# Optimization experiments

Measured on AMD Instinct MI355X. Metric: run time of the kernel, lower is better.

The kernel has to match this reference:

```python
import jax, jax.numpy as jnp
import numpy as np

DEPTH = 10
HID = 48
IN_DIM = 784
OUT_DIM = 10
STEPS = 20
LR = 0.1
BATCH = 65536


def setup_inputs() -> dict:
    key = jax.random.key(0)
    ks = jax.random.split(key, 8)
    x = jax.random.normal(ks[0], (BATCH, IN_DIM), dtype=jnp.float32)
    target = jax.random.randint(ks[1], (BATCH,), 0, OUT_DIM)
    W0 = jax.random.normal(ks[2], (HID, IN_DIM), dtype=jnp.float32) / np.sqrt(IN_DIM)
    b0 = jnp.zeros((HID,), dtype=jnp.float32)
    Wh = jax.random.normal(ks[3], (DEPTH - 1, HID, HID), dtype=jnp.float32) / np.sqrt(HID)
    bh = jnp.zeros((DEPTH - 1, HID), dtype=jnp.float32)
    Wout = jax.random.normal(ks[4], (OUT_DIM, HID), dtype=jnp.float32) / np.sqrt(HID)
    bout = jnp.zeros((OUT_DIM,), dtype=jnp.float32)
    return {"x": x, "target": target, "W0": W0, "b0": b0, "Wh": Wh, "bh": bh, "Wout": Wout, "bout": bout}


def _settle(x, target, W0, b0, Wh, bh, Wout, bout):
    # hidden-layer weights: weights[0] = (W0,b0); weights[i] = (Wh[i-1],bh[i-1]) for 1<=i<DEPTH;
    # output layer weights[DEPTH] = (Wout,bout)
    def hw(i):
        return (W0, b0) if i == 0 else (Wh[i - 1], bh[i - 1])

    # init value nodes with a standard forward pass
    vals = []
    h = x
    for i in range(DEPTH):
        Wi, bi = hw(i)
        h = jax.nn.relu(h @ Wi.T + bi)
        vals.append(h)
    V = jnp.stack(vals, 0)  # (DEPTH, B, HID) = v_1..v_DEPTH
    v_out = jax.nn.one_hot(target, OUT_DIM, dtype=jnp.float32)  # clamped output v_{DEPTH+1}

    def step(V, _):
        vs = [x] + [V[i] for i in range(DEPTH)] + [v_out]
        # prediction errors (computed once per settling step, from pre-step values)
        errors = []
        for i in range(DEPTH):
            Wi, bi = hw(i)
            pre = vs[i] @ Wi.T + bi
            errors.append(vs[i + 1] - jax.nn.relu(pre))
        errors.append(vs[DEPTH + 1] - (vs[DEPTH] @ Wout.T + bout))
        # value-node updates: dE/dv_i = eps_{i-1} - J_i^T eps_i
        new = []
        for i in range(1, DEPTH + 1):
            bu = errors[i - 1]
            if i < DEPTH:
                Wi, bi = hw(i)
                pre = vs[i] @ Wi.T + bi
                td = (errors[i] * (pre > 0).astype(pre.dtype)) @ Wi
            else:
                td = errors[DEPTH] @ Wout
            vi = vs[i] - LR * (bu - td)
            new.append(jnp.clip(vi, -10.0, 10.0))
        return jnp.stack(new, 0), None

    V, _ = jax.lax.scan(step, V, None, length=STEPS)
    return V  # (DEPTH, B, HID): settled hidden value nodes v_1..v_DEPTH


def reference(x, target, W0, b0, Wh, bh, Wout, bout):
    return _settle(x, target, W0, b0, Wh, bh, Wout, bout)
```

## Files before the change

### kernel.cpp

```cpp
#include <hip/hip_runtime.h>
#include <stdint.h>

typedef __attribute__((ext_vector_type(4))) _Float16 half4;
typedef __attribute__((ext_vector_type(2))) _Float16 h2;
typedef __attribute__((ext_vector_type(4))) float f32x4;
typedef __attribute__((ext_vector_type(2))) uint32_t uint2v;
typedef __attribute__((ext_vector_type(2))) short short2v;

#define BLOCK 512
#define MFMA16 __builtin_amdgcn_mfma_f32_16x16x16f16
#define SCHEDB __builtin_amdgcn_sched_barrier
#define PKRTZ  __builtin_amdgcn_cvt_pkrtz

#define TD_OFF    41472
#define BH_OFF    59904
#define LDS_BYTES 61632

extern __shared__ unsigned char smem[];

#define B32H(X) __builtin_bit_cast(uint32_t, (X))
#define H2U(X)  __builtin_bit_cast(h2, (X))

#define PACK4(S0,S1,S2,S3) __extension__({ \
  half4 _b; \
  _b[0] = (_Float16)(S0); _b[1] = (_Float16)(S1); \
  _b[2] = (_Float16)(S2); _b[3] = (_Float16)(S3); \
  _b; })
#define PACKU(S0,S1) __extension__({ \
  h2 _x; _x[0] = (_Float16)(S0); _x[1] = (_Float16)(S1); B32H(_x); })

#define VB(ROW, KS) __extension__({ \
  uint2v _u; _u[0] = (ROW)[2*(KS)]; _u[1] = (ROW)[2*(KS)+1]; \
  __builtin_bit_cast(half4, _u); })

#define TDA(I, ST) ((I) <= 5 \
  ? tdreg[(I) <= 5 ? (I)-1 : 0][ST] \
  : *(const half4*)(smem + TD_OFF + ((I) >= 6 ? (I)-6 : 0)*4608 + (ST)*512 + lane*8))

#define PRED48(SRCU, WOFF, LIDX, P0, P1, P2) do { \
  P0 = *(const f32x4*)(smem + BH_OFF + ((LIDX)*48 +  0)*4 + b*16); \
  P1 = *(const f32x4*)(smem + BH_OFF + ((LIDX)*48 + 16)*4 + b*16); \
  P2 = *(const f32x4*)(smem + BH_OFF + ((LIDX)*48 + 32)*4 + b*16); \
  _Pragma("unroll") \
  for (int _ks = 0; _ks < 3; ++_ks) { \
    half4 _B = VB(SRCU, _ks); \
    half4 _A0 = *(const half4*)(smem + (WOFF) + (0*3+_ks)*512 + lane*8); \
    half4 _A1 = *(const half4*)(smem + (WOFF) + (1*3+_ks)*512 + lane*8); \
    half4 _A2 = *(const half4*)(smem + (WOFF) + (2*3+_ks)*512 + lane*8); \
    P0 = MFMA16(_A0, _B, P0, 0, 0, 0); \
    P1 = MFMA16(_A1, _B, P1, 0, 0, 0); \
    P2 = MFMA16(_A2, _B, P2, 0, 0, 0); \
  } \
} while(0)

#define TD48(MEU, I, T0, T1, T2) do { \
  T0 = (f32x4){0.f,0.f,0.f,0.f}; T1 = T0; T2 = T0; \
  _Pragma("unroll") \
  for (int _ks = 0; _ks < 3; ++_ks) { \
    half4 _B = VB(MEU, _ks); \
    half4 _A0 = TDA(I, 0*3+_ks); \
    half4 _A1 = TDA(I, 1*3+_ks); \
    half4 _A2 = TDA(I, 2*3+_ks); \
    T0 = MFMA16(_A0, _B, T0, 0, 0, 0); \
    T1 = MFMA16(_A1, _B, T1, 0, 0, 0); \
    T2 = MFMA16(_A2, _B, T2, 0, 0, 0); \
  } \
} while(0)

#define PREP2(PLO, PHI, VU32, ERRU, MEU) do { \
  uint32_t _p = B32H(PKRTZ((PLO), (PHI))); \
  uint32_t _sm = __builtin_bit_cast(uint32_t, \
      (short2v)(__builtin_bit_cast(short2v, _p) >> 15)); \
  h2 _rl = __builtin_elementwise_max(H2U(_p), ZH2); \
  h2 _e = H2U(VU32) - _rl; \
  ERRU = B32H(_e); \
  MEU = ERRU & ~_sm; \
} while(0)

#define UPD2(TLO, THI, EPKU, VU, ERRU) do { \
  uint32_t _t = B32H(PKRTZ((TLO), (THI))); \
  h2 _d = H2U(EPKU) - H2U(_t); \
  h2 _nv = H2U(VU) - HLR2*_d; \
  _nv = __builtin_elementwise_min(__builtin_elementwise_max(_nv, NCLP2), PCLP2); \
  VU = B32H(_nv); \
  EPKU = ERRU; \
} while(0)

#define LAYER_STEP(I) do { \
  f32x4 _p0, _p1, _p2; \
  PRED48(vhu[(I)-1], ((I)-1)*4608, (I)-1, _p0, _p1, _p2); \
  uint32_t _err[6], _me[6]; \
  PREP2(_p0[0], _p0[1], vhu[I][0], _err[0], _me[0]); \
  PREP2(_p0[2], _p0[3], vhu[I][1], _err[1], _me[1]); \
  PREP2(_p1[0], _p1[1], vhu[I][2], _err[2], _me[2]); \
  PREP2(_p1[2], _p1[3], vhu[I][3], _err[3], _me[3]); \
  PREP2(_p2[0], _p2[1], vhu[I][4], _err[4], _me[4]); \
  PREP2(_p2[2], _p2[3], vhu[I][5], _err[5], _me[5]); \
  f32x4 _t0, _t1, _t2; \
  TD48(_me, I, _t0, _t1, _t2); \
  UPD2(_t0[0], _t0[1], epku[0], vhu[(I)-1][0], _err[0]); \
  UPD2(_t0[2], _t0[3], epku[1], vhu[(I)-1][1], _err[1]); \
  UPD2(_t1[0], _t1[1], epku[2], vhu[(I)-1][2], _err[2]); \
  UPD2(_t1[2], _t1[3], epku[3], vhu[(I)-1][3], _err[3]); \
  UPD2(_t2[0], _t2[1], epku[4], vhu[(I)-1][4], _err[4]); \
  UPD2(_t2[2], _t2[3], epku[5], vhu[(I)-1][5], _err[5]); \
} while(0)

#define FWD(I) do { \
  f32x4 _p0, _p1, _p2; \
  PRED48(vhu[(I)-1], ((I)-1)*4608, (I)-1, _p0, _p1, _p2); \
  vhu[I][0] = PACKU(fmaxf(_p0[0],0.f), fmaxf(_p0[1],0.f)); \
  vhu[I][1] = PACKU(fmaxf(_p0[2],0.f), fmaxf(_p0[3],0.f)); \
  vhu[I][2] = PACKU(fmaxf(_p1[0],0.f), fmaxf(_p1[1],0.f)); \
  vhu[I][3] = PACKU(fmaxf(_p1[2],0.f), fmaxf(_p1[3],0.f)); \
  vhu[I][4] = PACKU(fmaxf(_p2[0],0.f), fmaxf(_p2[1],0.f)); \
  vhu[I][5] = PACKU(fmaxf(_p2[2],0.f), fmaxf(_p2[3],0.f)); \
} while(0)

__global__ __launch_bounds__(BLOCK)
void pcnet_kernel(const float* __restrict__ x, const int* __restrict__ target,
                  const float* __restrict__ W0, const float* __restrict__ b0,
                  const float* __restrict__ Wh, const float* __restrict__ bh,
                  const float* __restrict__ Wout, const float* __restrict__ bout,
                  float* __restrict__ out)
{
    const int t = threadIdx.x;
    const int lane = t & 63;
    const int wv = t >> 6;
    const int n = lane & 15;
    const int b = lane >> 4;

    const int bsamp0 = blockIdx.x*128 + wv*16;
    const int samp = bsamp0 + n;

    const h2 HLR2  = (h2)(_Float16)0.1f;
    const h2 PCLP2 = (h2)(_Float16)10.0f;
    const h2 NCLP2 = (h2)(_Float16)(-10.0f);
    const h2 ZH2   = (h2)(_Float16)0.0f;

    f32x4 acc0[3];
    #pragma unroll
    for (int tm = 0; tm < 3; ++tm) acc0[tm] = (f32x4){0.f, 0.f, 0.f, 0.f};

    const float* xrow = x + (size_t)samp*784;
    for (int ch = 0; ch < 7; ++ch) {
        __syncthreads();
        for (int idx = t; idx < 1344; idx += BLOCK) {
            int st = idx >> 6, LB = idx & 63;
            int tm = st / 7, ksl = st - tm*7;
            int row = 16*tm + (LB & 15);
            int col = ch*112 + ksl*16 + 4*(LB >> 4);
            float4 w4 = *(const float4*)(W0 + row*784 + col);
            *(half4*)(smem + (tm*7+ksl)*512 + LB*8) = PACK4(w4.x, w4.y, w4.z, w4.w);
        }
        __syncthreads();
        #pragma unroll
        for (int ksl = 0; ksl < 7; ++ksl) {
            float4 xv = *(const float4*)(xrow + ch*112 + ksl*16 + 4*b);
            half4 xb = PACK4(xv.x, xv.y, xv.z, xv.w);
            #pragma unroll
            for (int tm = 0; tm < 3; ++tm) {
                half4 A = *(const half4*)(smem + (tm*7+ksl)*512 + lane*8);
                acc0[tm] = MFMA16(A, xb, acc0[tm], 0, 0, 0);
            }
        }
    }

    uint32_t vhu[10][6], a0u[6];
    #pragma unroll
    for (int tm = 0; tm < 3; ++tm) {
        float4 bb = *(const float4*)(b0 + 16*tm + 4*b);
        uint32_t lo = PACKU(fmaxf(acc0[tm][0] + bb.x, 0.f), fmaxf(acc0[tm][1] + bb.y, 0.f));
        uint32_t hi = PACKU(fmaxf(acc0[tm][2] + bb.z, 0.f), fmaxf(acc0[tm][3] + bb.w, 0.f));
        a0u[2*tm] = lo;   vhu[0][2*tm] = lo;
        a0u[2*tm+1] = hi; vhu[0][2*tm+1] = hi;
    }
    __syncthreads();

    for (int idx = t; idx < 5184; idx += BLOCK) {
        int L = idx / 576;
        int r2 = idx - L*576;
        int st = r2 >> 6, LB = r2 & 63;
        int tm = st / 3, ks = st - tm*3;
        int m  = 16*tm + (LB & 15);
        int k0 = 16*ks + 4*(LB >> 4);
        float4 w4 = *(const float4*)(Wh + L*2304 + m*48 + k0);
        *(half4*)(smem + L*4608 + st*512 + LB*8) = PACK4(w4.x, w4.y, w4.z, w4.w);
    }
    for (int idx = t; idx < 2304; idx += BLOCK) {
        int Lt = idx / 576;
        int r2 = idx - Lt*576;
        int st = r2 >> 6, LB = r2 & 63;
        int tm = st / 3, ks = st - tm*3;
        int m  = 16*tm + (LB & 15);
        int k0 = 16*ks + 4*(LB >> 4);
        const float* p = Wh + (Lt+5)*2304 + k0*48 + m;
        *(half4*)(smem + TD_OFF + Lt*4608 + st*512 + LB*8) = PACK4(p[0], p[48], p[96], p[144]);
    }
    for (int idx = t; idx < 432; idx += BLOCK)
        *(float*)(smem + BH_OFF + idx*4) = bh[idx];
    __syncthreads();

    half4 tdreg[5][9];
    #pragma unroll
    for (int L = 0; L < 5; ++L)
        #pragma unroll
        for (int st = 0; st < 9; ++st) {
            int tm = st / 3, ks = st - tm*3;
            int m  = 16*tm + (lane & 15);
            int k0 = 16*ks + 4*(lane >> 4);
            const float* p = Wh + L*2304 + k0*48 + m;
            tdreg[L][st] = PACK4(p[0], p[48], p[96], p[144]);
        }
    half4 WP[3], WT[3];
    {
        int c = lane & 15;
        #pragma unroll
        for (int ks = 0; ks < 3; ++ks) {
            if (c < 10) {
                float4 w4 = *(const float4*)(Wout + c*48 + 16*ks + 4*(lane >> 4));
                WP[ks] = PACK4(w4.x, w4.y, w4.z, w4.w);
            } else {
                WP[ks] = PACK4(0.f, 0.f, 0.f, 0.f);
            }
        }
        int c0 = 4*(lane >> 4);
        #pragma unroll
        for (int tm = 0; tm < 3; ++tm) {
            int m = 16*tm + (lane & 15);
            float w0 = (c0+0 < 10) ? Wout[(c0+0)*48 + m] : 0.f;
            float w1 = (c0+1 < 10) ? Wout[(c0+1)*48 + m] : 0.f;
            float w2 = (c0+2 < 10) ? Wout[(c0+2)*48 + m] : 0.f;
            float w3 = (c0+3 < 10) ? Wout[(c0+3)*48 + m] : 0.f;
            WT[tm] = PACK4(w0, w1, w2, w3);
        }
    }
    f32x4 bo4;
    #pragma unroll
    for (int q = 0; q < 4; ++q) bo4[q] = (4*b+q < 10) ? bout[4*b+q] : 0.f;
    const int tg = target[samp];

    FWD(1); FWD(2); FWD(3); FWD(4); FWD(5); FWD(6); FWD(7); FWD(8); FWD(9);
    SCHEDB(0);

    #pragma unroll 1
    for (int s = 0; s < 20; ++s) {
        uint32_t epku[6];
        #pragma unroll
        for (int j = 0; j < 6; ++j)
            epku[j] = B32H(H2U(vhu[0][j]) - H2U(a0u[j]));

        LAYER_STEP(1); LAYER_STEP(2); LAYER_STEP(3);
        SCHEDB(0);
        LAYER_STEP(4); LAYER_STEP(5); LAYER_STEP(6);
        SCHEDB(0);
        LAYER_STEP(7); LAYER_STEP(8); LAYER_STEP(9);
        SCHEDB(0);

        {
            f32x4 accP = bo4;
            #pragma unroll
            for (int ks = 0; ks < 3; ++ks)
                accP = MFMA16(WP[ks], VB(vhu[9], ks), accP, 0, 0, 0);
            int c0 = 4*b;
            float e0 = (c0+0 < 10) ? (((c0+0 == tg) ? 1.f : 0.f) - accP[0]) : 0.f;
            float e1 = (c0+1 < 10) ? (((c0+1 == tg) ? 1.f : 0.f) - accP[1]) : 0.f;
            float e2 = (c0+2 < 10) ? (((c0+2 == tg) ? 1.f : 0.f) - accP[2]) : 0.f;
            float e3 = (c0+3 < 10) ? (((c0+3 == tg) ? 1.f : 0.f) - accP[3]) : 0.f;
            uint32_t eBu[2];
            eBu[0] = B32H(PKRTZ(e0, e1));
            eBu[1] = B32H(PKRTZ(e2, e3));
            half4 eB = VB(eBu, 0);
            #pragma unroll
            for (int tm = 0; tm < 3; ++tm) {
                f32x4 a2 = {0.f, 0.f, 0.f, 0.f};
                a2 = MFMA16(WT[tm], eB, a2, 0, 0, 0);
                {
                    uint32_t _t = B32H(PKRTZ(a2[0], a2[1]));
                    h2 _d = H2U(epku[2*tm]) - H2U(_t);
                    h2 _nv = H2U(vhu[9][2*tm]) - HLR2*_d;
                    _nv = __builtin_elementwise_min(__builtin_elementwise_max(_nv, NCLP2), PCLP2);
                    vhu[9][2*tm] = B32H(_nv);
                }
                {
                    uint32_t _t = B32H(PKRTZ(a2[2], a2[3]));
                    h2 _d = H2U(epku[2*tm+1]) - H2U(_t);
                    h2 _nv = H2U(vhu[9][2*tm+1]) - HLR2*_d;
                    _nv = __builtin_elementwise_min(__builtin_elementwise_max(_nv, NCLP2), PCLP2);
                    vhu[9][2*tm+1] = B32H(_nv);
                }
            }
            SCHEDB(0);
        }
    }

    #pragma unroll
    for (int L2 = 0; L2 < 10; ++L2) {
        #pragma unroll
        for (int tt = 0; tt < 3; ++tt) {
            h2 lo = H2U(vhu[L2][2*tt]);
            h2 hi = H2U(vhu[L2][2*tt+1]);
            f32x4 w4 = { (float)lo[0], (float)lo[1], (float)hi[0], (float)hi[1] };
            *(f32x4*)(out + (size_t)L2*65536*48 + (size_t)samp*48 + tt*16 + 4*b) = w4;
        }
    }
}

extern "C" void kernel_launch(void* const* d_in, const int* in_sizes, int n_in,
                              void* d_out, int out_size, void* d_ws, size_t ws_size,
                              hipStream_t stream) {
    const float* x      = (const float*)d_in[0];
    const int*   target = (const int*)d_in[1];
    const float* W0     = (const float*)d_in[2];
    const float* b0     = (const float*)d_in[3];
    const float* Wh     = (const float*)d_in[4];
    const float* bh     = (const float*)d_in[5];
    const float* Wout   = (const float*)d_in[6];
    const float* bout   = (const float*)d_in[7];
    float* out = (float*)d_out;

    hipFuncSetAttribute((const void*)pcnet_kernel,
                        hipFuncAttributeMaxDynamicSharedMemorySize, LDS_BYTES);

    dim3 grid(65536/128);
    dim3 block(BLOCK);
    pcnet_kernel<<<grid, block, LDS_BYTES, stream>>>(x, target, W0, b0, Wh, bh, Wout, bout, out);
}
```

Before: 277.4 us.

## Use 16x16x32 MFMA with permuted hidden layout for 48-wide layer GEMMs

Replaces the three 16x16x16 MFMA k-steps per 48-wide tile with two 16x16x32 MFMAs. Each K=32 fragment holds 24 real values plus zero padding, so each lane's 12 hidden values map directly to B fragments. Hidden units are permuted (row = 12*(r>>2)+4*tm+(r&3)) so each lane owns 12 contiguous units, and W0, biases, Wout and the output store are remapped to match. All transposed weights now live in LDS, removing the register-held tdreg copies. This cuts MFMA instruction count and register pressure, at the cost of a larger LDS footprint (about 112KB) and a third of the MFMA work spent on zero padding.

```diff
diff --git a/kernel.cpp b/kernel.cpp
--- a/kernel.cpp
+++ b/kernel.cpp
@@ -2,19 +2,23 @@
 #include <stdint.h>
 
 typedef __attribute__((ext_vector_type(4))) _Float16 half4;
+typedef __attribute__((ext_vector_type(8))) _Float16 half8;
 typedef __attribute__((ext_vector_type(2))) _Float16 h2;
 typedef __attribute__((ext_vector_type(4))) float f32x4;
 typedef __attribute__((ext_vector_type(2))) uint32_t uint2v;
+typedef __attribute__((ext_vector_type(4))) uint32_t uint4v;
 typedef __attribute__((ext_vector_type(2))) short short2v;
 
 #define BLOCK 512
 #define MFMA16 __builtin_amdgcn_mfma_f32_16x16x16f16
+#define MFMA32 __builtin_amdgcn_mfma_f32_16x16x32_f16
 #define SCHEDB __builtin_amdgcn_sched_barrier
 #define PKRTZ  __builtin_amdgcn_cvt_pkrtz
 
-#define TD_OFF    41472
-#define BH_OFF    59904
-#define LDS_BYTES 61632
+#define PRED_OFF  0
+#define TD_OFF    55296
+#define BH_OFF    110592
+#define LDS_BYTES 112320
 
 extern __shared__ unsigned char smem[];
 
@@ -33,37 +37,40 @@
   uint2v _u; _u[0] = (ROW)[2*(KS)]; _u[1] = (ROW)[2*(KS)+1]; \
   __builtin_bit_cast(half4, _u); })
 
-#define TDA(I, ST) ((I) <= 5 \
-  ? tdreg[(I) <= 5 ? (I)-1 : 0][ST] \
-  : *(const half4*)(smem + TD_OFF + ((I) >= 6 ? (I)-6 : 0)*4608 + (ST)*512 + lane*8))
-
-#define PRED48(SRCU, WOFF, LIDX, P0, P1, P2) do { \
-  P0 = *(const f32x4*)(smem + BH_OFF + ((LIDX)*48 +  0)*4 + b*16); \
-  P1 = *(const f32x4*)(smem + BH_OFF + ((LIDX)*48 + 16)*4 + b*16); \
-  P2 = *(const f32x4*)(smem + BH_OFF + ((LIDX)*48 + 32)*4 + b*16); \
+#define BFRAG(SRCU, KS) __extension__({ \
+  uint4v _u; _u[0] = (SRCU)[3*(KS)]; _u[1] = (SRCU)[3*(KS)+1]; \
+  _u[2] = (SRCU)[3*(KS)+2]; _u[3] = 0u; \
+  __builtin_bit_cast(half8, _u); })
+
+#define PRED48(SRCU, LAY, P0, P1, P2) do { \
+  const unsigned char* _wb = smem + PRED_OFF + (LAY)*6144; \
+  P0 = *(const f32x4*)(smem + BH_OFF + ((LAY)*48 + 12*b + 0)*4); \
+  P1 = *(const f32x4*)(smem + BH_OFF + ((LAY)*48 + 12*b + 4)*4); \
+  P2 = *(const f32x4*)(smem + BH_OFF + ((LAY)*48 + 12*b + 8)*4); \
   _Pragma("unroll") \
-  for (int _ks = 0; _ks < 3; ++_ks) { \
-    half4 _B = VB(SRCU, _ks); \
-    half4 _A0 = *(const half4*)(smem + (WOFF) + (0*3+_ks)*512 + lane*8); \
-    half4 _A1 = *(const half4*)(smem + (WOFF) + (1*3+_ks)*512 + lane*8); \
-    half4 _A2 = *(const half4*)(smem + (WOFF) + (2*3+_ks)*512 + lane*8); \
-    P0 = MFMA16(_A0, _B, P0, 0, 0, 0); \
-    P1 = MFMA16(_A1, _B, P1, 0, 0, 0); \
-    P2 = MFMA16(_A2, _B, P2, 0, 0, 0); \
+  for (int _ks = 0; _ks < 2; ++_ks) { \
+    half8 _B = BFRAG(SRCU, _ks); \
+    half8 _A0 = *(const half8*)(_wb + (0*2+_ks)*1024 + lane*16); \
+    half8 _A1 = *(const half8*)(_wb + (1*2+_ks)*1024 + lane*16); \
+    half8 _A2 = *(const half8*)(_wb + (2*2+_ks)*1024 + lane*16); \
+    P0 = MFMA32(_A0, _B, P0, 0, 0, 0); \
+    P1 = MFMA32(_A1, _B, P1, 0, 0, 0); \
+    P2 = MFMA32(_A2, _B, P2, 0, 0, 0); \
   } \
 } while(0)
 
-#define TD48(MEU, I, T0, T1, T2) do { \
+#define TD48(MEU, LAY, T0, T1, T2) do { \
+  const unsigned char* _wb = smem + TD_OFF + (LAY)*6144; \
   T0 = (f32x4){0.f,0.f,0.f,0.f}; T1 = T0; T2 = T0; \
   _Pragma("unroll") \
-  for (int _ks = 0; _ks < 3; ++_ks) { \
-    half4 _B = VB(MEU, _ks); \
-    half4 _A0 = TDA(I, 0*3+_ks); \
-    half4 _A1 = TDA(I, 1*3+_ks); \
-    half4 _A2 = TDA(I, 2*3+_ks); \
-    T0 = MFMA16(_A0, _B, T0, 0, 0, 0); \
-    T1 = MFMA16(_A1, _B, T1, 0, 0, 0); \
-    T2 = MFMA16(_A2, _B, T2, 0, 0, 0); \
+  for (int _ks = 0; _ks < 2; ++_ks) { \
+    half8 _B = BFRAG(MEU, _ks); \
+    half8 _A0 = *(const half8*)(_wb + (0*2+_ks)*1024 + lane*16); \
+    half8 _A1 = *(const half8*)(_wb + (1*2+_ks)*1024 + lane*16); \
+    half8 _A2 = *(const half8*)(_wb + (2*2+_ks)*1024 + lane*16); \
+    T0 = MFMA32(_A0, _B, T0, 0, 0, 0); \
+    T1 = MFMA32(_A1, _B, T1, 0, 0, 0); \
+    T2 = MFMA32(_A2, _B, T2, 0, 0, 0); \
   } \
 } while(0)
 
@@ -88,7 +95,7 @@
 
 #define LAYER_STEP(I) do { \
   f32x4 _p0, _p1, _p2; \
-  PRED48(vhu[(I)-1], ((I)-1)*4608, (I)-1, _p0, _p1, _p2); \
+  PRED48(vhu[(I)-1], (I)-1, _p0, _p1, _p2); \
   uint32_t _err[6], _me[6]; \
   PREP2(_p0[0], _p0[1], vhu[I][0], _err[0], _me[0]); \
   PREP2(_p0[2], _p0[3], vhu[I][1], _err[1], _me[1]); \
@@ -97,7 +104,7 @@
   PREP2(_p2[0], _p2[1], vhu[I][4], _err[4], _me[4]); \
   PREP2(_p2[2], _p2[3], vhu[I][5], _err[5], _me[5]); \
   f32x4 _t0, _t1, _t2; \
-  TD48(_me, I, _t0, _t1, _t2); \
+  TD48(_me, (I)-1, _t0, _t1, _t2); \
   UPD2(_t0[0], _t0[1], epku[0], vhu[(I)-1][0], _err[0]); \
   UPD2(_t0[2], _t0[3], epku[1], vhu[(I)-1][1], _err[1]); \
   UPD2(_t1[0], _t1[1], epku[2], vhu[(I)-1][2], _err[2]); \
@@ -108,7 +115,7 @@
 
 #define FWD(I) do { \
   f32x4 _p0, _p1, _p2; \
-  PRED48(vhu[(I)-1], ((I)-1)*4608, (I)-1, _p0, _p1, _p2); \
+  PRED48(vhu[(I)-1], (I)-1, _p0, _p1, _p2); \
   vhu[I][0] = PACKU(fmaxf(_p0[0],0.f), fmaxf(_p0[1],0.f)); \
   vhu[I][1] = PACKU(fmaxf(_p0[2],0.f), fmaxf(_p0[3],0.f)); \
   vhu[I][2] = PACKU(fmaxf(_p1[0],0.f), fmaxf(_p1[1],0.f)); \
@@ -148,7 +155,8 @@
         for (int idx = t; idx < 1344; idx += BLOCK) {
             int st = idx >> 6, LB = idx & 63;
             int tm = st / 7, ksl = st - tm*7;
-            int row = 16*tm + (LB & 15);
+            int r = LB & 15;
+            int row = 12*(r>>2) + 4*tm + (r&3);
             int col = ch*112 + ksl*16 + 4*(LB >> 4);
             float4 w4 = *(const float4*)(W0 + row*784 + col);
             *(half4*)(smem + (tm*7+ksl)*512 + LB*8) = PACK4(w4.x, w4.y, w4.z, w4.w);
@@ -169,7 +177,7 @@
     uint32_t vhu[10][6], a0u[6];
     #pragma unroll
     for (int tm = 0; tm < 3; ++tm) {
-        float4 bb = *(const float4*)(b0 + 16*tm + 4*b);
+        float4 bb = *(const float4*)(b0 + 12*b + 4*tm);
         uint32_t lo = PACKU(fmaxf(acc0[tm][0] + bb.x, 0.f), fmaxf(acc0[tm][1] + bb.y, 0.f));
         uint32_t hi = PACKU(fmaxf(acc0[tm][2] + bb.z, 0.f), fmaxf(acc0[tm][3] + bb.w, 0.f));
         a0u[2*tm] = lo;   vhu[0][2*tm] = lo;
@@ -177,57 +185,55 @@
     }
     __syncthreads();
 
-    for (int idx = t; idx < 5184; idx += BLOCK) {
-        int L = idx / 576;
-        int r2 = idx - L*576;
+    for (int idx = t; idx < 3456; idx += BLOCK) {
+        int L = idx / 384;
+        int r2 = idx - L*384;
         int st = r2 >> 6, LB = r2 & 63;
-        int tm = st / 3, ks = st - tm*3;
-        int m  = 16*tm + (LB & 15);
-        int k0 = 16*ks + 4*(LB >> 4);
-        float4 w4 = *(const float4*)(Wh + L*2304 + m*48 + k0);
-        *(half4*)(smem + L*4608 + st*512 + LB*8) = PACK4(w4.x, w4.y, w4.z, w4.w);
-    }
-    for (int idx = t; idx < 2304; idx += BLOCK) {
-        int Lt = idx / 576;
-        int r2 = idx - Lt*576;
+        int tm = st >> 1, ks = st & 1;
+        int r = LB & 15, g = LB >> 4;
+        int row = 12*(r>>2) + 4*tm + (r&3);
+        int c0 = 12*g + 6*ks;
+        const float* p = Wh + L*2304 + row*48 + c0;
+        uint4v w;
+        w[0] = PACKU(p[0], p[1]); w[1] = PACKU(p[2], p[3]);
+        w[2] = PACKU(p[4], p[5]); w[3] = 0u;
+        *(uint4v*)(smem + PRED_OFF + L*6144 + st*1024 + LB*16) = w;
+    }
+    for (int idx = t; idx < 3456; idx += BLOCK) {
+        int L = idx / 384;
+        int r2 = idx - L*384;
         int st = r2 >> 6, LB = r2 & 63;
-        int tm = st / 3, ks = st - tm*3;
-        int m  = 16*tm + (LB & 15);
-        int k0 = 16*ks + 4*(LB >> 4);
-        const float* p = Wh + (Lt+5)*2304 + k0*48 + m;
-        *(half4*)(smem + TD_OFF + Lt*4608 + st*512 + LB*8) = PACK4(p[0], p[48], p[96], p[144]);
+        int tm = st >> 1, ks = st & 1;
+        int r = LB & 15, g = LB >> 4;
+        int row = 12*(r>>2) + 4*tm + (r&3);
+        int c0 = 12*g + 6*ks;
+        const float* p = Wh + L*2304 + c0*48 + row;
+        uint4v w;
+        w[0] = PACKU(p[0], p[48]); w[1] = PACKU(p[96], p[144]);
+        w[2] = PACKU(p[192], p[240]); w[3] = 0u;
+        *(uint4v*)(smem + TD_OFF + L*6144 + st*1024 + LB*16) = w;
     }
     for (int idx = t; idx < 432; idx += BLOCK)
         *(float*)(smem + BH_OFF + idx*4) = bh[idx];
     __syncthreads();
 
-    half4 tdreg[5][9];
-    #pragma unroll
-    for (int L = 0; L < 5; ++L)
-        #pragma unroll
-        for (int st = 0; st < 9; ++st) {
-            int tm = st / 3, ks = st - tm*3;
-            int m  = 16*tm + (lane & 15);
-            int k0 = 16*ks + 4*(lane >> 4);
-            const float* p = Wh + L*2304 + k0*48 + m;
-            tdreg[L][st] = PACK4(p[0], p[48], p[96], p[144]);
-        }
     half4 WP[3], WT[3];
     {
-        int c = lane & 15;
+        int c = lane & 15, g = lane >> 4;
         #pragma unroll
         for (int ks = 0; ks < 3; ++ks) {
             if (c < 10) {
-                float4 w4 = *(const float4*)(Wout + c*48 + 16*ks + 4*(lane >> 4));
+                float4 w4 = *(const float4*)(Wout + c*48 + 12*g + 4*ks);
                 WP[ks] = PACK4(w4.x, w4.y, w4.z, w4.w);
             } else {
                 WP[ks] = PACK4(0.f, 0.f, 0.f, 0.f);
             }
         }
-        int c0 = 4*(lane >> 4);
+        int r = lane & 15;
+        int c0 = 4*g;
         #pragma unroll
         for (int tm = 0; tm < 3; ++tm) {
-            int m = 16*tm + (lane & 15);
+            int m = 12*(r>>2) + 4*tm + (r&3);
             float w0 = (c0+0 < 10) ? Wout[(c0+0)*48 + m] : 0.f;
             float w1 = (c0+1 < 10) ? Wout[(c0+1)*48 + m] : 0.f;
             float w2 = (c0+2 < 10) ? Wout[(c0+2)*48 + m] : 0.f;
@@ -301,7 +307,7 @@
             h2 lo = H2U(vhu[L2][2*tt]);
             h2 hi = H2U(vhu[L2][2*tt+1]);
             f32x4 w4 = { (float)lo[0], (float)lo[1], (float)hi[0], (float)hi[1] };
-            *(f32x4*)(out + (size_t)L2*65536*48 + (size_t)samp*48 + tt*16 + 4*b) = w4;
+            *(f32x4*)(out + (size_t)L2*65536*48 + (size_t)samp*48 + 12*b + 4*tt) = w4;
         }
     }
 }
```

After: 268.3 us. -3.3%, faster.
